# Optimization experiments

Measured on AMD Instinct MI355X. Metric: run time of the kernel, lower is better.

Reference implementation:

```python
import jax, jax.numpy as jnp
import numpy as np

N = 200000
D = 128
B = 8
VS = 0.4
XMIN, YMIN, ZMIN = -50.0, -50.0, -5.0
NX, NY, NZ = 250, 250, 20
VXYZ = NX * NY * NZ
FILL = np.int32(2_000_000_000)  # > any real voxel key, so padded uniques sort last
BN_EPS = 1e-5


def _bn(x, g, b, m, v):
    # BatchNorm1d in eval mode with given running stats
    return (x - m) * jax.lax.rsqrt(v + BN_EPS) * g + b


def _leaky(x):
    return jnp.where(x >= 0, x, 0.1 * x)


def setup_inputs() -> dict:
    key = jax.random.key(0)
    ks = jax.random.split(key, 12)
    points_feature = jax.random.normal(ks[0], (N, D), jnp.float32)
    u = jax.random.uniform(ks[1], (N, 3), jnp.float32)
    lo = jnp.array([XMIN, YMIN, ZMIN], jnp.float32)
    ext = jnp.array([100.0, 100.0, 8.0], jnp.float32)
    points_center = lo + 0.001 + u * (ext - 0.002)  # strictly inside pc_range
    batch_idx = jax.random.randint(ks[2], (N,), 0, B, jnp.int32)
    foreground_mask = jax.random.randint(ks[3], (N,), 0, 2, jnp.int32).astype(bool)
    timestamp = jax.random.normal(ks[4], (B,), jnp.float32) * 0.1
    w_pf = jax.random.normal(ks[5], (3 * D, D), jnp.float32) / np.sqrt(3 * D)
    b_pf = jax.random.normal(ks[6], (D,), jnp.float32) * 0.01
    g_pf = jax.random.uniform(ks[7], (D,), jnp.float32) + 0.5
    be_pf = jax.random.normal(ks[8], (D,), jnp.float32) * 0.1
    m_pf = jax.random.normal(ks[9], (D,), jnp.float32) * 0.1
    v_pf = jax.random.uniform(ks[10], (D,), jnp.float32) + 0.5
    ks2 = jax.random.split(ks[11], 6)
    w_cp = jax.random.normal(ks2[0], (D, D), jnp.float32) / np.sqrt(D)
    b_cp = jax.random.normal(ks2[1], (D,), jnp.float32) * 0.01
    g_cp = jax.random.uniform(ks2[2], (D,), jnp.float32) + 0.5
    be_cp = jax.random.normal(ks2[3], (D,), jnp.float32) * 0.1
    m_cp = jax.random.normal(ks2[4], (D,), jnp.float32) * 0.1
    v_cp = jax.random.uniform(ks2[5], (D,), jnp.float32) + 0.5
    return dict(points_feature=points_feature, points_center=points_center,
                batch_idx=batch_idx, foreground_mask=foreground_mask,
                timestamp=timestamp,
                w_pf=w_pf, b_pf=b_pf, g_pf=g_pf, be_pf=be_pf, m_pf=m_pf, v_pf=v_pf,
                w_cp=w_cp, b_cp=b_cp, g_cp=g_cp, be_cp=be_cp, m_cp=m_cp, v_cp=v_cp)


def reference(points_feature, points_center, batch_idx, foreground_mask, timestamp,
              w_pf, b_pf, g_pf, be_pf, m_pf, v_pf,
              w_cp, b_cp, g_cp, be_cp, m_cp, v_cp):
    # NOTE: the original forward computes a time position embedding and then
    # overwrites it with zeros_like, so its net contribution is exactly zero.
    n = points_feature.shape[0]
    # voxelize point centers -> (b, xi, yi, zi) encoded as a single int key
    xi = jnp.floor((points_center[:, 0] - XMIN) / VS).astype(jnp.int32)
    yi = jnp.floor((points_center[:, 1] - YMIN) / VS).astype(jnp.int32)
    zi = jnp.floor((points_center[:, 2] - ZMIN) / VS).astype(jnp.int32)
    vkey = ((batch_idx.astype(jnp.int32) * NX + xi) * NY + yi) * NZ + zi
    # torch.unique(dim=0) sorts lexicographically == sorted scalar keys
    uk, inv = jnp.unique(vkey, return_inverse=True, size=n, fill_value=FILL)
    fgf = foreground_mask.astype(points_feature.dtype)
    # K = points_cluster_idx_fore.max() + 1 (number of foreground clusters)
    K = jnp.max(jnp.where(foreground_mask, inv, -1)) + 1
    # scatter_mean of foreground point features per cluster (empty -> 0)
    cnt = jax.ops.segment_sum(fgf, inv, num_segments=n)
    csum = jax.ops.segment_sum(points_feature * fgf[:, None], inv, num_segments=n)
    cmean = csum / jnp.maximum(cnt, 1.0)[:, None]
    proj = _leaky(_bn(cmean @ w_cp + b_cp, g_cp, be_cp, m_cp, v_cp))
    valid = jnp.arange(n) < K
    # cluster_feature_all: rows < K hold projected cluster features, rest are 0
    cfa = jnp.where(valid[:, None], proj, 0.0)
    # associate voxels: halve the batch id (agent pairing), re-unique
    akey = (uk // VXYZ // 2) * VXYZ + uk % VXYZ
    _, ainv = jnp.unique(akey, return_inverse=True, size=n, fill_value=FILL)
    # scatter_mean of cluster features over associate voxels (only valid clusters)
    acnt = jax.ops.segment_sum(valid.astype(points_feature.dtype), ainv, num_segments=n)
    asum = jax.ops.segment_sum(cfa, ainv, num_segments=n)
    amean = asum / jnp.maximum(acnt, 1.0)[:, None]
    pf_assoc = amean[ainv[inv]]   # gather per point via voxel -> associate id
    pf_clu = cfa[inv]             # gather per point cluster feature
    amask = (pf_clu - pf_assoc).sum(axis=1) > 0
    cat = jnp.concatenate([points_feature, pf_clu, pf_assoc], axis=1)
    h = _leaky(_bn(cat @ w_pf + b_pf, g_pf, be_pf, m_pf, v_pf))
    newf = jnp.where(amask[:, None], h, points_feature)
    # original early-returns points_feature if associate_mask.sum() <= 1
    return jnp.where(amask.sum() > 1, newf, points_feature)
```

## Files before the change

kernel.cpp:

```cpp
#include <hip/hip_runtime.h>

#define SCAN_BS 256
#define SCAN_IT 16
#define SCAN_CHUNK (SCAN_BS * SCAN_IT)
#define NVOX 10000000
#define NAVOX 5000000
#define VXYZK 1250000

__device__ __forceinline__ float leakyf(float x) { return x >= 0.0f ? x : 0.1f * x; }

__global__ void k_init(int* c) {
  int t = threadIdx.x;
  if (t < 8) c[t] = (t == 2) ? -1 : 0;
}

__global__ void k_detect_fg(const unsigned* __restrict__ w, int nw, int* __restrict__ c) {
  int i = blockIdx.x * blockDim.x + threadIdx.x;
  if (i < nw && w[i] > 1u) atomicOr(&c[4], 1);
}

__device__ __forceinline__ int fg_get(const void* fgp, int i, int mode) {
  return mode ? (((const unsigned char*)fgp)[i] != 0) : (((const int*)fgp)[i] != 0);
}

__global__ void k_vkey(const float* __restrict__ pc, const int* __restrict__ bidx,
                       int* __restrict__ vkey, unsigned* __restrict__ dense, int N) {
  int i = blockIdx.x * blockDim.x + threadIdx.x;
  if (i >= N) return;
  float x = pc[3 * i], y = pc[3 * i + 1], z = pc[3 * i + 2];
  int xi = (int)floorf((x - (-50.0f)) / 0.4f);
  int yi = (int)floorf((y - (-50.0f)) / 0.4f);
  int zi = (int)floorf((z - (-5.0f)) / 0.4f);
  xi = min(max(xi, 0), 249); yi = min(max(yi, 0), 249); zi = min(max(zi, 0), 19);
  int b = min(max(bidx[i], 0), 7);
  int key = ((b * 250 + xi) * 250 + yi) * 20 + zi;
  vkey[i] = key;
  dense[key] = 1u;
}

__global__ void k_scan_block(unsigned* __restrict__ data, int n, unsigned* __restrict__ bsums) {
  __shared__ unsigned s[SCAN_BS];
  int tid = threadIdx.x;
  long base = (long)blockIdx.x * SCAN_CHUNK + (long)tid * SCAN_IT;
  unsigned v[SCAN_IT];
  unsigned tsum = 0;
#pragma unroll
  for (int j = 0; j < SCAN_IT; ++j) {
    long idx = base + j;
    v[j] = (idx < (long)n) ? data[idx] : 0u;
    tsum += v[j];
  }
  unsigned x = tsum;
  s[tid] = x;
  for (int off = 1; off < SCAN_BS; off <<= 1) {
    __syncthreads();
    unsigned y = (tid >= off) ? s[tid - off] : 0u;
    __syncthreads();
    x += y;
    s[tid] = x;
  }
  if (tid == SCAN_BS - 1) bsums[blockIdx.x] = x;
  unsigned run = x - tsum;
#pragma unroll
  for (int j = 0; j < SCAN_IT; ++j) {
    long idx = base + j;
    if (idx < (long)n) { data[idx] = run; run += v[j]; }
  }
}

__global__ void k_scan_sums(unsigned* __restrict__ data, int n, int* __restrict__ totalOut) {
  __shared__ unsigned s[SCAN_BS];
  int tid = threadIdx.x;
  int base = tid * SCAN_IT;
  unsigned v[SCAN_IT];
  unsigned tsum = 0;
#pragma unroll
  for (int j = 0; j < SCAN_IT; ++j) {
    int idx = base + j;
    v[j] = (idx < n) ? data[idx] : 0u;
    tsum += v[j];
  }
  unsigned x = tsum;
  s[tid] = x;
  for (int off = 1; off < SCAN_BS; off <<= 1) {
    __syncthreads();
    unsigned y = (tid >= off) ? s[tid - off] : 0u;
    __syncthreads();
    x += y;
    s[tid] = x;
  }
  if (tid == SCAN_BS - 1) *totalOut = (int)x;
  unsigned run = x - tsum;
#pragma unroll
  for (int j = 0; j < SCAN_IT; ++j) {
    int idx = base + j;
    if (idx < n) { data[idx] = run; run += v[j]; }
  }
}

__global__ void k_inv_ukey(const int* __restrict__ vkey, const unsigned* __restrict__ dense,
                           const unsigned* __restrict__ bsums, const void* __restrict__ fgp,
                           int* __restrict__ inv, int* __restrict__ ukey,
                           int* __restrict__ c, int N) {
  int i = blockIdx.x * blockDim.x + threadIdx.x;
  if (i >= N) return;
  int k = vkey[i];
  int r = (int)(dense[k] + bsums[k >> 12]);
  inv[i] = r;
  ukey[r] = k;
  if (fg_get(fgp, i, c[4])) atomicMax(&c[2], r);
}

__global__ void k_akey_mark(const int* __restrict__ ukey, int* __restrict__ akey,
                            unsigned* __restrict__ dense, const int* __restrict__ c, int N) {
  int r = blockIdx.x * blockDim.x + threadIdx.x;
  if (r >= N || r >= c[0]) return;
  int uk = ukey[r];
  int ak = (uk / VXYZK / 2) * VXYZK + uk % VXYZK;
  akey[r] = ak;
  dense[ak] = 1u;
}

__global__ void k_ainv(const int* __restrict__ akey, const unsigned* __restrict__ dense,
                       const unsigned* __restrict__ bsums, int* __restrict__ ainv,
                       const int* __restrict__ c, int N) {
  int r = blockIdx.x * blockDim.x + threadIdx.x;
  if (r >= N || r >= c[0]) return;
  int ak = akey[r];
  ainv[r] = (int)(dense[ak] + bsums[ak >> 12]);
}

__global__ void k_gcnt(const int* __restrict__ ainv_u, unsigned* __restrict__ gcnt,
                       const int* __restrict__ c, int N) {
  int r = blockIdx.x * blockDim.x + threadIdx.x;
  if (r >= N || r >= c[0]) return;
  atomicAdd(&gcnt[ainv_u[r]], 1u);
}

__global__ void k_build_lists(const int* __restrict__ ainv_u, const unsigned* __restrict__ gcnt,
                              int* __restrict__ mlist, int* __restrict__ nlist,
                              unsigned char* __restrict__ needp, int* __restrict__ c, int N) {
  int r = blockIdx.x * blockDim.x + threadIdx.x;
  if (r >= N || r >= c[0]) return;
  int g = ainv_u[r];
  if (gcnt[g] >= 2u) {
    int mp = atomicAdd(&c[5], 1);
    mlist[mp] = r;
    if (r <= c[2]) {
      needp[r] = 1;
      int np = atomicAdd(&c[6], 1);
      nlist[np] = r;
    }
  }
}

__global__ void k_zero_rows(const int* __restrict__ mlist, const int* __restrict__ ainv_u,
                            const int* __restrict__ c, float* __restrict__ csum,
                            float* __restrict__ asum) {
  int total = c[5] * 128;
  int stride = gridDim.x * blockDim.x;
  for (int idx = blockIdx.x * blockDim.x + threadIdx.x; idx < total; idx += stride) {
    int r = mlist[idx >> 7];
    int d = idx & 127;
    asum[(size_t)ainv_u[r] * 128 + d] = 0.0f;
    if (r <= c[2]) csum[(size_t)r * 128 + d] = 0.0f;
  }
}

__global__ void k_point_filter(const void* __restrict__ fgp, const int* __restrict__ inv,
                               const unsigned char* __restrict__ needp, float* __restrict__ cnt,
                               int* __restrict__ clist, int* __restrict__ c, int N) {
  int i = blockIdx.x * blockDim.x + threadIdx.x;
  if (i >= N) return;
  if (!fg_get(fgp, i, c[4])) return;
  int r = inv[i];
  if (!needp[r]) return;
  atomicAdd(&cnt[r], 1.0f);
  int p = atomicAdd(&c[7], 1);
  clist[p] = i;
}

__global__ void k_csum_accum(const float* __restrict__ pf, const int* __restrict__ clist,
                             const int* __restrict__ inv, float* __restrict__ csum,
                             const int* __restrict__ c) {
  int total = c[7] * 128;
  int stride = gridDim.x * blockDim.x;
  for (int idx = blockIdx.x * blockDim.x + threadIdx.x; idx < total; idx += stride) {
    int i = clist[idx >> 7];
    int d = idx & 127;
    int r = inv[i];
    atomicAdd(&csum[(size_t)r * 128 + d], pf[(size_t)i * 128 + d]);
  }
}

__global__ __launch_bounds__(128) void k_proj16(
    float* __restrict__ cs, const float* __restrict__ cnt, const int* __restrict__ nlist,
    const float* __restrict__ W, const float* __restrict__ bb,
    const float* __restrict__ gg, const float* __restrict__ be,
    const float* __restrict__ mm, const float* __restrict__ vv, const int* __restrict__ c) {
  int nc = c[6];
  int ntiles = (nc + 15) >> 4;
  __shared__ __align__(16) float tile[16][128];
  __shared__ int srow[16];
  int d = threadIdx.x;
  for (int tb = blockIdx.x; tb < ntiles; tb += gridDim.x) {
    int base = tb * 16;
    if (d < 16) srow[d] = (base + d < nc) ? nlist[base + d] : -1;
    __syncthreads();
    for (int p = 0; p < 16; ++p) {
      int r = srow[p];
      tile[p][d] = (r >= 0) ? cs[(size_t)r * 128 + d] / fmaxf(cnt[r], 1.0f) : 0.0f;
    }
    __syncthreads();
    float acc[16];
#pragma unroll
    for (int p = 0; p < 16; ++p) acc[p] = 0.0f;
    for (int k4 = 0; k4 < 32; ++k4) {
      float w0 = W[(4 * k4 + 0) * 128 + d];
      float w1 = W[(4 * k4 + 1) * 128 + d];
      float w2 = W[(4 * k4 + 2) * 128 + d];
      float w3 = W[(4 * k4 + 3) * 128 + d];
#pragma unroll
      for (int p = 0; p < 16; ++p) {
        float4 t4 = *(const float4*)&tile[p][4 * k4];
        acc[p] = fmaf(t4.x, w0, acc[p]);
        acc[p] = fmaf(t4.y, w1, acc[p]);
        acc[p] = fmaf(t4.z, w2, acc[p]);
        acc[p] = fmaf(t4.w, w3, acc[p]);
      }
    }
    float biasd = bb[d], scale = gg[d] / sqrtf(vv[d] + 1e-5f), md = mm[d], bed = be[d];
    for (int p = 0; p < 16; ++p) {
      int r = srow[p];
      if (r >= 0) {
        float pre = acc[p] + biasd;
        cs[(size_t)r * 128 + d] = leakyf((pre - md) * scale + bed);
      }
    }
    __syncthreads();
  }
}

__global__ void k_asum_accum(const float* __restrict__ cs, const int* __restrict__ nlist,
                             const int* __restrict__ ainv_u, float* __restrict__ asum,
                             float* __restrict__ acnt, const int* __restrict__ c) {
  int total = c[6] * 128;
  int stride = gridDim.x * blockDim.x;
  for (int idx = blockIdx.x * blockDim.x + threadIdx.x; idx < total; idx += stride) {
    int r = nlist[idx >> 7];
    int d = idx & 127;
    int g = ainv_u[r];
    atomicAdd(&asum[(size_t)g * 128 + d], cs[(size_t)r * 128 + d]);
    if (d == 0) atomicAdd(&acnt[g], 1.0f);
  }
}

__global__ void k_amask2(const float* __restrict__ cs, const float* __restrict__ asum,
                         const float* __restrict__ acnt, const int* __restrict__ ainv_u,
                         const int* __restrict__ mlist, const int* __restrict__ c,
                         unsigned* __restrict__ flag) {
  int mcount = c[5];
  int groups = gridDim.x * (blockDim.x >> 6);
  int j0 = blockIdx.x * (blockDim.x >> 6) + (threadIdx.x >> 6);
  int lane = threadIdx.x & 63;
  for (int j = j0; j < mcount; j += groups) {
    int r = mlist[j];
    int g = ainv_u[r];
    float mc = fmaxf(acnt[g], 1.0f);
    bool valid = r <= c[2];
    size_t rb = (size_t)r * 128, gb = (size_t)g * 128;
    float c0 = valid ? cs[rb + lane] : 0.0f;
    float c1 = valid ? cs[rb + 64 + lane] : 0.0f;
    float s = (c0 - asum[gb + lane] / mc) + (c1 - asum[gb + 64 + lane] / mc);
    for (int off = 32; off > 0; off >>= 1) s += __shfl_down(s, off);
    if (lane == 0) flag[r] = (s > 0.0f) ? 1u : 0u;
  }
}

__global__ void k_flagpts(const int* __restrict__ inv, const unsigned* __restrict__ flag,
                          int* __restrict__ plist, int* __restrict__ c, int N) {
  int i = blockIdx.x * blockDim.x + threadIdx.x;
  if (i >= N) return;
  if (flag[inv[i]]) {
    int p = atomicAdd(&c[3], 1);
    plist[p] = i;
  }
}

__global__ void k_copy(const float* __restrict__ pf, float* __restrict__ out, long n4) {
  long stride = (long)gridDim.x * blockDim.x;
  for (long idx = (long)blockIdx.x * blockDim.x + threadIdx.x; idx < n4; idx += stride) {
    ((float4*)out)[idx] = ((const float4*)pf)[idx];
  }
}

__global__ __launch_bounds__(128) void k_fgemm(
    const float* __restrict__ pf, const float* __restrict__ cs,
    const float* __restrict__ asum, const float* __restrict__ acnt,
    const int* __restrict__ inv, const int* __restrict__ ainv_u,
    const int* __restrict__ plist, const int* __restrict__ c,
    const float* __restrict__ W, const float* __restrict__ bb,
    const float* __restrict__ gg, const float* __restrict__ be,
    const float* __restrict__ mm, const float* __restrict__ vv,
    float* __restrict__ out) {
  int pcnt = c[3];
  if (pcnt <= 1) return;
  int ntiles = (pcnt + 15) >> 4;
  __shared__ __align__(16) float tile[16][384];
  __shared__ int si[16], sr[16], sg[16];
  __shared__ float smc[16];
  int t = threadIdx.x;
  int kmax = c[2];
  for (int tb = blockIdx.x; tb < ntiles; tb += gridDim.x) {
    int base = tb * 16;
    if (t < 16) {
      int i = (base + t < pcnt) ? plist[base + t] : -1;
      si[t] = i;
      int r = (i >= 0) ? inv[i] : 0;
      sr[t] = r;
      int g = ainv_u[r];
      sg[t] = g;
      smc[t] = fmaxf(acnt[g], 1.0f);
    }
    __syncthreads();
    for (int e = t; e < 16 * 96; e += 128) {
      int p = e / 96, f4 = e % 96;
      int i = si[p];
      float4 v = make_float4(0.f, 0.f, 0.f, 0.f);
      if (i >= 0) {
        if (f4 < 32) {
          v = ((const float4*)pf)[(size_t)i * 32 + f4];
        } else if (f4 < 64) {
          int r = sr[p];
          if (r <= kmax) v = ((const float4*)cs)[(size_t)r * 32 + (f4 - 32)];
        } else {
          float4 a = ((const float4*)asum)[(size_t)sg[p] * 32 + (f4 - 64)];
          float mc = smc[p];
          v = make_float4(a.x / mc, a.y / mc, a.z / mc, a.w / mc);
        }
      }
      *(float4*)&tile[p][f4 * 4] = v;
    }
    __syncthreads();
    float acc[16];
#pragma unroll
    for (int p = 0; p < 16; ++p) acc[p] = 0.0f;
    for (int k4 = 0; k4 < 96; ++k4) {
      float w0 = W[(4 * k4 + 0) * 128 + t];
      float w1 = W[(4 * k4 + 1) * 128 + t];
      float w2 = W[(4 * k4 + 2) * 128 + t];
      float w3 = W[(4 * k4 + 3) * 128 + t];
#pragma unroll
      for (int p = 0; p < 16; ++p) {
        float4 t4 = *(const float4*)&tile[p][4 * k4];
        acc[p] = fmaf(t4.x, w0, acc[p]);
        acc[p] = fmaf(t4.y, w1, acc[p]);
        acc[p] = fmaf(t4.z, w2, acc[p]);
        acc[p] = fmaf(t4.w, w3, acc[p]);
      }
    }
    float biasd = bb[t], scale = gg[t] / sqrtf(vv[t] + 1e-5f), md = mm[t], bed = be[t];
    for (int p = 0; p < 16; ++p) {
      int i = si[p];
      if (i >= 0) {
        float pre = acc[p] + biasd;
        out[(size_t)i * 128 + t] = leakyf((pre - md) * scale + bed);
      }
    }
    __syncthreads();
  }
}

extern "C" void kernel_launch(void* const* d_in, const int* in_sizes, int n_in,
                              void* d_out, int out_size, void* d_ws, size_t ws_size,
                              hipStream_t stream) {
  (void)n_in; (void)out_size; (void)ws_size;
  const float* pf   = (const float*)d_in[0];
  const float* pc   = (const float*)d_in[1];
  const int*   bidx = (const int*)d_in[2];
  const void*  fgp  = d_in[3];
  const float* Wpf  = (const float*)d_in[5];
  const float* bpf  = (const float*)d_in[6];
  const float* gpf  = (const float*)d_in[7];
  const float* bepf = (const float*)d_in[8];
  const float* mpf  = (const float*)d_in[9];
  const float* vpf  = (const float*)d_in[10];
  const float* Wcp  = (const float*)d_in[11];
  const float* bcp  = (const float*)d_in[12];
  const float* gcp  = (const float*)d_in[13];
  const float* becp = (const float*)d_in[14];
  const float* mcp  = (const float*)d_in[15];
  const float* vcp  = (const float*)d_in[16];
  float* out = (float*)d_out;
  int N = in_sizes[0] / 128;

  char* ws = (char*)d_ws;
  size_t o = 0;
  auto take = [&](size_t bytes) -> void* {
    void* p = ws + o;
    o += (bytes + 255) & ~(size_t)255;
    return p;
  };
  unsigned* dense  = (unsigned*)take((size_t)NVOX * 4);
  int* vkey        = (int*)take((size_t)N * 4);
  int* inv         = (int*)take((size_t)N * 4);
  int* ukey        = (int*)take((size_t)N * 4);
  int* akey        = (int*)take((size_t)N * 4);
  int* ainv_u      = (int*)take((size_t)N * 4);
  float* cnt       = (float*)take((size_t)N * 4);
  float* acnt      = (float*)take((size_t)N * 4);
  unsigned* flag   = (unsigned*)take((size_t)N * 4);
  unsigned* gcnt   = (unsigned*)take((size_t)N * 4);
  int* nlist       = (int*)take((size_t)N * 4);
  int* clist       = (int*)take((size_t)N * 4);
  unsigned char* needp = (unsigned char*)take((size_t)N);
  unsigned* bsums1 = (unsigned*)take((size_t)4096 * 4);
  unsigned* bsums2 = (unsigned*)take((size_t)4096 * 4);
  int* ctr         = (int*)take(256);
  float* csum      = (float*)take((size_t)N * 128 * 4);
  float* asum      = (float*)take((size_t)N * 128 * 4);
  int* mlist = vkey;
  int* plist = akey;

  hipMemsetAsync(dense, 0, (size_t)NVOX * 4, stream);
  hipMemsetAsync(cnt, 0, (size_t)N * 4, stream);
  hipMemsetAsync(acnt, 0, (size_t)N * 4, stream);
  hipMemsetAsync(flag, 0, (size_t)N * 4, stream);
  hipMemsetAsync(gcnt, 0, (size_t)N * 4, stream);
  hipMemsetAsync(needp, 0, (size_t)N, stream);
  k_init<<<1, 64, 0, stream>>>(ctr);

  int nb = (N + 255) / 256;
  int nw = N / 4;
  k_detect_fg<<<(nw + 255) / 256, 256, 0, stream>>>((const unsigned*)fgp, nw, ctr);
  k_vkey<<<nb, 256, 0, stream>>>(pc, bidx, vkey, dense, N);

  int blk1 = (NVOX + SCAN_CHUNK - 1) / SCAN_CHUNK;
  k_scan_block<<<blk1, SCAN_BS, 0, stream>>>(dense, NVOX, bsums1);
  k_scan_sums<<<1, SCAN_BS, 0, stream>>>(bsums1, blk1, &ctr[0]);
  k_inv_ukey<<<nb, 256, 0, stream>>>(vkey, dense, bsums1, fgp, inv, ukey, ctr, N);

  hipMemsetAsync(dense, 0, (size_t)NAVOX * 4, stream);
  k_akey_mark<<<nb, 256, 0, stream>>>(ukey, akey, dense, ctr, N);
  int blk2 = (NAVOX + SCAN_CHUNK - 1) / SCAN_CHUNK;
  k_scan_block<<<blk2, SCAN_BS, 0, stream>>>(dense, NAVOX, bsums2);
  k_scan_sums<<<1, SCAN_BS, 0, stream>>>(bsums2, blk2, &ctr[1]);
  k_ainv<<<nb, 256, 0, stream>>>(akey, dense, bsums2, ainv_u, ctr, N);

  k_gcnt<<<nb, 256, 0, stream>>>(ainv_u, gcnt, ctr, N);
  k_build_lists<<<nb, 256, 0, stream>>>(ainv_u, gcnt, mlist, nlist, needp, ctr, N);

  int gsw = 3125;
  k_zero_rows<<<gsw, 256, 0, stream>>>(mlist, ainv_u, ctr, csum, asum);
  k_point_filter<<<nb, 256, 0, stream>>>(fgp, inv, needp, cnt, clist, ctr, N);
  k_csum_accum<<<gsw, 256, 0, stream>>>(pf, clist, inv, csum, ctr);
  k_proj16<<<gsw, 128, 0, stream>>>(csum, cnt, nlist, Wcp, bcp, gcp, becp, mcp, vcp, ctr);
  k_asum_accum<<<gsw, 256, 0, stream>>>(csum, nlist, ainv_u, asum, acnt, ctr);
  k_amask2<<<1024, 256, 0, stream>>>(csum, asum, acnt, ainv_u, mlist, ctr, flag);
  k_flagpts<<<nb, 256, 0, stream>>>(inv, flag, plist, ctr, N);

  long n4 = (long)N * 32;
  k_copy<<<12800, 256, 0, stream>>>(pf, out, n4);
  k_fgemm<<<gsw, 128, 0, stream>>>(pf, csum, asum, acnt, inv, ainv_u, plist, ctr,
                                   Wpf, bpf, gpf, bepf, mpf, vpf, out);
}
```

Baseline: 582.2 us.

## Replace dense voxel occupancy arrays with bitsets and fuse small kernels

Voxel occupancy moves from 40MB/20MB dense uint arrays to bitsets with popcount-based word prefix scans and rank lookups. This shrinks the memset and scan traffic considerably. Several small kernels are fused: fg detection into vkey, gcnt into ainv, zero_rows with point_filter, and flagpts with copy. Memsets are collapsed into one contiguous region, the per-thread fg atomicMax becomes a wave reduction, and grid sizes are retuned.

After: 466.0 us. 20.0% less time.

```diff
diff --git a/kernel.cpp b/kernel.cpp
--- a/kernel.cpp
+++ b/kernel.cpp
@@ -5,27 +5,22 @@
 #define SCAN_CHUNK (SCAN_BS * SCAN_IT)
 #define NVOX 10000000
 #define NAVOX 5000000
+#define NWORDS1 312500
+#define NWORDS2 156250
 #define VXYZK 1250000
 
 __device__ __forceinline__ float leakyf(float x) { return x >= 0.0f ? x : 0.1f * x; }
-
-__global__ void k_init(int* c) {
-  int t = threadIdx.x;
-  if (t < 8) c[t] = (t == 2) ? -1 : 0;
-}
-
-__global__ void k_detect_fg(const unsigned* __restrict__ w, int nw, int* __restrict__ c) {
-  int i = blockIdx.x * blockDim.x + threadIdx.x;
-  if (i < nw && w[i] > 1u) atomicOr(&c[4], 1);
-}
 
 __device__ __forceinline__ int fg_get(const void* fgp, int i, int mode) {
   return mode ? (((const unsigned char*)fgp)[i] != 0) : (((const int*)fgp)[i] != 0);
 }
 
 __global__ void k_vkey(const float* __restrict__ pc, const int* __restrict__ bidx,
-                       int* __restrict__ vkey, unsigned* __restrict__ dense, int N) {
+                       const unsigned* __restrict__ fgw, int nw,
+                       int* __restrict__ vkey, unsigned* __restrict__ bits,
+                       int* __restrict__ c, int N) {
   int i = blockIdx.x * blockDim.x + threadIdx.x;
+  if (i < nw && fgw[i] > 1u) atomicOr(&c[4], 1);
   if (i >= N) return;
   float x = pc[3 * i], y = pc[3 * i + 1], z = pc[3 * i + 2];
   int xi = (int)floorf((x - (-50.0f)) / 0.4f);
@@ -35,10 +30,11 @@
   int b = min(max(bidx[i], 0), 7);
   int key = ((b * 250 + xi) * 250 + yi) * 20 + zi;
   vkey[i] = key;
-  dense[key] = 1u;
-}
-
-__global__ void k_scan_block(unsigned* __restrict__ data, int n, unsigned* __restrict__ bsums) {
+  atomicOr(&bits[key >> 5], 1u << (key & 31));
+}
+
+__global__ void k_scan_pop(const unsigned* __restrict__ bits, int nwords,
+                           unsigned* __restrict__ wordpfx, unsigned* __restrict__ bsums) {
   __shared__ unsigned s[SCAN_BS];
   int tid = threadIdx.x;
   long base = (long)blockIdx.x * SCAN_CHUNK + (long)tid * SCAN_IT;
@@ -47,7 +43,7 @@
 #pragma unroll
   for (int j = 0; j < SCAN_IT; ++j) {
     long idx = base + j;
-    v[j] = (idx < (long)n) ? data[idx] : 0u;
+    v[j] = (idx < (long)nwords) ? (unsigned)__popc(bits[idx]) : 0u;
     tsum += v[j];
   }
   unsigned x = tsum;
@@ -64,7 +60,7 @@
 #pragma unroll
   for (int j = 0; j < SCAN_IT; ++j) {
     long idx = base + j;
-    if (idx < (long)n) { data[idx] = run; run += v[j]; }
+    if (idx < (long)nwords) { wordpfx[idx] = run; run += v[j]; }
   }
 }
 
@@ -98,43 +94,50 @@
   }
 }
 
-__global__ void k_inv_ukey(const int* __restrict__ vkey, const unsigned* __restrict__ dense,
-                           const unsigned* __restrict__ bsums, const void* __restrict__ fgp,
-                           int* __restrict__ inv, int* __restrict__ ukey,
-                           int* __restrict__ c, int N) {
+__device__ __forceinline__ int rank_of(int key, const unsigned* bits,
+                                       const unsigned* wordpfx, const unsigned* bsums) {
+  int w = key >> 5, b = key & 31;
+  return (int)(wordpfx[w] + bsums[w >> 12] + (unsigned)__popc(bits[w] & ((1u << b) - 1u)));
+}
+
+__global__ void k_inv_ukey(const int* __restrict__ vkey, const unsigned* __restrict__ bits,
+                           const unsigned* __restrict__ wordpfx, const unsigned* __restrict__ bsums,
+                           const void* __restrict__ fgp, int* __restrict__ inv,
+                           int* __restrict__ ukey, int* __restrict__ c, int N) {
   int i = blockIdx.x * blockDim.x + threadIdx.x;
-  if (i >= N) return;
-  int k = vkey[i];
-  int r = (int)(dense[k] + bsums[k >> 12]);
-  inv[i] = r;
-  ukey[r] = k;
-  if (fg_get(fgp, i, c[4])) atomicMax(&c[2], r);
+  bool valid = i < N;
+  int mode = c[4];
+  int r = 0;
+  if (valid) {
+    int k = vkey[i];
+    r = rank_of(k, bits, wordpfx, bsums);
+    inv[i] = r;
+    ukey[r] = k;
+  }
+  int fgr = (valid && fg_get(fgp, i, mode)) ? r : -1;
+  for (int off = 32; off > 0; off >>= 1) fgr = max(fgr, __shfl_down(fgr, off));
+  if ((threadIdx.x & 63) == 0 && fgr >= 0) atomicMax(&c[2], fgr + 1);
 }
 
 __global__ void k_akey_mark(const int* __restrict__ ukey, int* __restrict__ akey,
-                            unsigned* __restrict__ dense, const int* __restrict__ c, int N) {
+                            unsigned* __restrict__ abits, const int* __restrict__ c, int N) {
   int r = blockIdx.x * blockDim.x + threadIdx.x;
   if (r >= N || r >= c[0]) return;
   int uk = ukey[r];
   int ak = (uk / VXYZK / 2) * VXYZK + uk % VXYZK;
   akey[r] = ak;
-  dense[ak] = 1u;
-}
-
-__global__ void k_ainv(const int* __restrict__ akey, const unsigned* __restrict__ dense,
-                       const unsigned* __restrict__ bsums, int* __restrict__ ainv,
+  atomicOr(&abits[ak >> 5], 1u << (ak & 31));
+}
+
+__global__ void k_ainv(const int* __restrict__ akey, const unsigned* __restrict__ abits,
+                       const unsigned* __restrict__ awordpfx, const unsigned* __restrict__ bsums,
+                       int* __restrict__ ainv, unsigned* __restrict__ gcnt,
                        const int* __restrict__ c, int N) {
   int r = blockIdx.x * blockDim.x + threadIdx.x;
   if (r >= N || r >= c[0]) return;
-  int ak = akey[r];
-  ainv[r] = (int)(dense[ak] + bsums[ak >> 12]);
-}
-
-__global__ void k_gcnt(const int* __restrict__ ainv_u, unsigned* __restrict__ gcnt,
-                       const int* __restrict__ c, int N) {
-  int r = blockIdx.x * blockDim.x + threadIdx.x;
-  if (r >= N || r >= c[0]) return;
-  atomicAdd(&gcnt[ainv_u[r]], 1u);
+  int g = rank_of(akey[r], abits, awordpfx, bsums);
+  ainv[r] = g;
+  atomicAdd(&gcnt[g], 1u);
 }
 
 __global__ void k_build_lists(const int* __restrict__ ainv_u, const unsigned* __restrict__ gcnt,
@@ -142,11 +145,10 @@
                               unsigned char* __restrict__ needp, int* __restrict__ c, int N) {
   int r = blockIdx.x * blockDim.x + threadIdx.x;
   if (r >= N || r >= c[0]) return;
-  int g = ainv_u[r];
-  if (gcnt[g] >= 2u) {
+  if (gcnt[ainv_u[r]] >= 2u) {
     int mp = atomicAdd(&c[5], 1);
     mlist[mp] = r;
-    if (r <= c[2]) {
+    if (r < c[2]) {
       needp[r] = 1;
       int np = atomicAdd(&c[6], 1);
       nlist[np] = r;
@@ -154,30 +156,31 @@
   }
 }
 
-__global__ void k_zero_rows(const int* __restrict__ mlist, const int* __restrict__ ainv_u,
-                            const int* __restrict__ c, float* __restrict__ csum,
-                            float* __restrict__ asum) {
-  int total = c[5] * 128;
+__global__ void k_zero_filter(const int* __restrict__ mlist, const int* __restrict__ ainv_u,
+                              const void* __restrict__ fgp, const int* __restrict__ inv,
+                              const unsigned char* __restrict__ needp,
+                              float* __restrict__ csum, float* __restrict__ asum,
+                              float* __restrict__ cnt, int* __restrict__ clist,
+                              int* __restrict__ c, int N) {
   int stride = gridDim.x * blockDim.x;
-  for (int idx = blockIdx.x * blockDim.x + threadIdx.x; idx < total; idx += stride) {
+  int tid0 = blockIdx.x * blockDim.x + threadIdx.x;
+  int K = c[2];
+  int totalA = c[5] * 128;
+  for (int idx = tid0; idx < totalA; idx += stride) {
     int r = mlist[idx >> 7];
     int d = idx & 127;
     asum[(size_t)ainv_u[r] * 128 + d] = 0.0f;
-    if (r <= c[2]) csum[(size_t)r * 128 + d] = 0.0f;
-  }
-}
-
-__global__ void k_point_filter(const void* __restrict__ fgp, const int* __restrict__ inv,
-                               const unsigned char* __restrict__ needp, float* __restrict__ cnt,
-                               int* __restrict__ clist, int* __restrict__ c, int N) {
-  int i = blockIdx.x * blockDim.x + threadIdx.x;
-  if (i >= N) return;
-  if (!fg_get(fgp, i, c[4])) return;
-  int r = inv[i];
-  if (!needp[r]) return;
-  atomicAdd(&cnt[r], 1.0f);
-  int p = atomicAdd(&c[7], 1);
-  clist[p] = i;
+    if (r < K) csum[(size_t)r * 128 + d] = 0.0f;
+  }
+  int mode = c[4];
+  for (int i = tid0; i < N; i += stride) {
+    if (!fg_get(fgp, i, mode)) continue;
+    int r = inv[i];
+    if (!needp[r]) continue;
+    atomicAdd(&cnt[r], 1.0f);
+    int p = atomicAdd(&c[7], 1);
+    clist[p] = i;
+  }
 }
 
 __global__ void k_csum_accum(const float* __restrict__ pf, const int* __restrict__ clist,
@@ -188,8 +191,7 @@
   for (int idx = blockIdx.x * blockDim.x + threadIdx.x; idx < total; idx += stride) {
     int i = clist[idx >> 7];
     int d = idx & 127;
-    int r = inv[i];
-    atomicAdd(&csum[(size_t)r * 128 + d], pf[(size_t)i * 128 + d]);
+    atomicAdd(&csum[(size_t)inv[i] * 128 + d], pf[(size_t)i * 128 + d]);
   }
 }
 
@@ -263,11 +265,12 @@
   int groups = gridDim.x * (blockDim.x >> 6);
   int j0 = blockIdx.x * (blockDim.x >> 6) + (threadIdx.x >> 6);
   int lane = threadIdx.x & 63;
+  int K = c[2];
   for (int j = j0; j < mcount; j += groups) {
     int r = mlist[j];
     int g = ainv_u[r];
     float mc = fmaxf(acnt[g], 1.0f);
-    bool valid = r <= c[2];
+    bool valid = r < K;
     size_t rb = (size_t)r * 128, gb = (size_t)g * 128;
     float c0 = valid ? cs[rb + lane] : 0.0f;
     float c1 = valid ? cs[rb + 64 + lane] : 0.0f;
@@ -277,19 +280,19 @@
   }
 }
 
-__global__ void k_flagpts(const int* __restrict__ inv, const unsigned* __restrict__ flag,
-                          int* __restrict__ plist, int* __restrict__ c, int N) {
-  int i = blockIdx.x * blockDim.x + threadIdx.x;
-  if (i >= N) return;
-  if (flag[inv[i]]) {
-    int p = atomicAdd(&c[3], 1);
-    plist[p] = i;
-  }
-}
-
-__global__ void k_copy(const float* __restrict__ pf, float* __restrict__ out, long n4) {
+__global__ void k_copy_flag(const float* __restrict__ pf, const int* __restrict__ inv,
+                            const unsigned* __restrict__ flag, float* __restrict__ out,
+                            int* __restrict__ plist, int* __restrict__ c, int N) {
   long stride = (long)gridDim.x * blockDim.x;
-  for (long idx = (long)blockIdx.x * blockDim.x + threadIdx.x; idx < n4; idx += stride) {
+  long tid0 = (long)blockIdx.x * blockDim.x + threadIdx.x;
+  for (long i = tid0; i < (long)N; i += stride) {
+    if (flag[inv[i]]) {
+      int p = atomicAdd(&c[3], 1);
+      plist[p] = (int)i;
+    }
+  }
+  long n4 = (long)N * 32;
+  for (long idx = tid0; idx < n4; idx += stride) {
     ((float4*)out)[idx] = ((const float4*)pf)[idx];
   }
 }
@@ -305,12 +308,12 @@
     float* __restrict__ out) {
   int pcnt = c[3];
   if (pcnt <= 1) return;
+  int K = c[2];
   int ntiles = (pcnt + 15) >> 4;
   __shared__ __align__(16) float tile[16][384];
   __shared__ int si[16], sr[16], sg[16];
   __shared__ float smc[16];
   int t = threadIdx.x;
-  int kmax = c[2];
   for (int tb = blockIdx.x; tb < ntiles; tb += gridDim.x) {
     int base = tb * 16;
     if (t < 16) {
@@ -332,7 +335,7 @@
           v = ((const float4*)pf)[(size_t)i * 32 + f4];
         } else if (f4 < 64) {
           int r = sr[p];
-          if (r <= kmax) v = ((const float4*)cs)[(size_t)r * 32 + (f4 - 32)];
+          if (r < K) v = ((const float4*)cs)[(size_t)r * 32 + (f4 - 32)];
         } else {
           float4 a = ((const float4*)asum)[(size_t)sg[p] * 32 + (f4 - 64)];
           float mc = smc[p];
@@ -401,66 +404,57 @@
     o += (bytes + 255) & ~(size_t)255;
     return p;
   };
-  unsigned* dense  = (unsigned*)take((size_t)NVOX * 4);
+  unsigned* bits   = (unsigned*)take((size_t)NWORDS1 * 4);
+  unsigned* abits  = (unsigned*)take((size_t)NWORDS2 * 4);
+  float* cnt       = (float*)take((size_t)N * 4);
+  float* acnt      = (float*)take((size_t)N * 4);
+  unsigned* flag   = (unsigned*)take((size_t)N * 4);
+  unsigned* gcnt   = (unsigned*)take((size_t)N * 4);
+  unsigned char* needp = (unsigned char*)take((size_t)N);
+  int* ctr         = (int*)take(256);
+  size_t zeroBytes = o;
+  unsigned* wordpfx  = (unsigned*)take((size_t)NWORDS1 * 4);
+  unsigned* awordpfx = (unsigned*)take((size_t)NWORDS2 * 4);
+  unsigned* bsums1 = (unsigned*)take((size_t)4096 * 4);
+  unsigned* bsums2 = (unsigned*)take((size_t)4096 * 4);
   int* vkey        = (int*)take((size_t)N * 4);
   int* inv         = (int*)take((size_t)N * 4);
   int* ukey        = (int*)take((size_t)N * 4);
   int* akey        = (int*)take((size_t)N * 4);
   int* ainv_u      = (int*)take((size_t)N * 4);
-  float* cnt       = (float*)take((size_t)N * 4);
-  float* acnt      = (float*)take((size_t)N * 4);
-  unsigned* flag   = (unsigned*)take((size_t)N * 4);
-  unsigned* gcnt   = (unsigned*)take((size_t)N * 4);
   int* nlist       = (int*)take((size_t)N * 4);
   int* clist       = (int*)take((size_t)N * 4);
-  unsigned char* needp = (unsigned char*)take((size_t)N);
-  unsigned* bsums1 = (unsigned*)take((size_t)4096 * 4);
-  unsigned* bsums2 = (unsigned*)take((size_t)4096 * 4);
-  int* ctr         = (int*)take(256);
   float* csum      = (float*)take((size_t)N * 128 * 4);
   float* asum      = (float*)take((size_t)N * 128 * 4);
   int* mlist = vkey;
   int* plist = akey;
 
-  hipMemsetAsync(dense, 0, (size_t)NVOX * 4, stream);
-  hipMemsetAsync(cnt, 0, (size_t)N * 4, stream);
-  hipMemsetAsync(acnt, 0, (size_t)N * 4, stream);
-  hipMemsetAsync(flag, 0, (size_t)N * 4, stream);
-  hipMemsetAsync(gcnt, 0, (size_t)N * 4, stream);
-  hipMemsetAsync(needp, 0, (size_t)N, stream);
-  k_init<<<1, 64, 0, stream>>>(ctr);
+  hipMemsetAsync(ws, 0, zeroBytes, stream);
 
   int nb = (N + 255) / 256;
   int nw = N / 4;
-  k_detect_fg<<<(nw + 255) / 256, 256, 0, stream>>>((const unsigned*)fgp, nw, ctr);
-  k_vkey<<<nb, 256, 0, stream>>>(pc, bidx, vkey, dense, N);
-
-  int blk1 = (NVOX + SCAN_CHUNK - 1) / SCAN_CHUNK;
-  k_scan_block<<<blk1, SCAN_BS, 0, stream>>>(dense, NVOX, bsums1);
+  k_vkey<<<nb, 256, 0, stream>>>(pc, bidx, (const unsigned*)fgp, nw, vkey, bits, ctr, N);
+
+  int blk1 = (NWORDS1 + SCAN_CHUNK - 1) / SCAN_CHUNK;
+  k_scan_pop<<<blk1, SCAN_BS, 0, stream>>>(bits, NWORDS1, wordpfx, bsums1);
   k_scan_sums<<<1, SCAN_BS, 0, stream>>>(bsums1, blk1, &ctr[0]);
-  k_inv_ukey<<<nb, 256, 0, stream>>>(vkey, dense, bsums1, fgp, inv, ukey, ctr, N);
-
-  hipMemsetAsync(dense, 0, (size_t)NAVOX * 4, stream);
-  k_akey_mark<<<nb, 256, 0, stream>>>(ukey, akey, dense, ctr, N);
-  int blk2 = (NAVOX + SCAN_CHUNK - 1) / SCAN_CHUNK;
-  k_scan_block<<<blk2, SCAN_BS, 0, stream>>>(dense, NAVOX, bsums2);
+  k_inv_ukey<<<nb, 256, 0, stream>>>(vkey, bits, wordpfx, bsums1, fgp, inv, ukey, ctr, N);
+
+  k_akey_mark<<<nb, 256, 0, stream>>>(ukey, akey, abits, ctr, N);
+  int blk2 = (NWORDS2 + SCAN_CHUNK - 1) / SCAN_CHUNK;
+  k_scan_pop<<<blk2, SCAN_BS, 0, stream>>>(abits, NWORDS2, awordpfx, bsums2);
   k_scan_sums<<<1, SCAN_BS, 0, stream>>>(bsums2, blk2, &ctr[1]);
-  k_ainv<<<nb, 256, 0, stream>>>(akey, dense, bsums2, ainv_u, ctr, N);
-
-  k_gcnt<<<nb, 256, 0, stream>>>(ainv_u, gcnt, ctr, N);
+  k_ainv<<<nb, 256, 0, stream>>>(akey, abits, awordpfx, bsums2, ainv_u, gcnt, ctr, N);
+
   k_build_lists<<<nb, 256, 0, stream>>>(ainv_u, gcnt, mlist, nlist, needp, ctr, N);
-
-  int gsw = 3125;
-  k_zero_rows<<<gsw, 256, 0, stream>>>(mlist, ainv_u, ctr, csum, asum);
-  k_point_filter<<<nb, 256, 0, stream>>>(fgp, inv, needp, cnt, clist, ctr, N);
-  k_csum_accum<<<gsw, 256, 0, stream>>>(pf, clist, inv, csum, ctr);
-  k_proj16<<<gsw, 128, 0, stream>>>(csum, cnt, nlist, Wcp, bcp, gcp, becp, mcp, vcp, ctr);
-  k_asum_accum<<<gsw, 256, 0, stream>>>(csum, nlist, ainv_u, asum, acnt, ctr);
-  k_amask2<<<1024, 256, 0, stream>>>(csum, asum, acnt, ainv_u, mlist, ctr, flag);
-  k_flagpts<<<nb, 256, 0, stream>>>(inv, flag, plist, ctr, N);
-
-  long n4 = (long)N * 32;
-  k_copy<<<12800, 256, 0, stream>>>(pf, out, n4);
-  k_fgemm<<<gsw, 128, 0, stream>>>(pf, csum, asum, acnt, inv, ainv_u, plist, ctr,
-                                   Wpf, bpf, gpf, bepf, mpf, vpf, out);
-}
+  k_zero_filter<<<1024, 256, 0, stream>>>(mlist, ainv_u, fgp, inv, needp,
+                                          csum, asum, cnt, clist, ctr, N);
+  k_csum_accum<<<1024, 256, 0, stream>>>(pf, clist, inv, csum, ctr);
+  k_proj16<<<512, 128, 0, stream>>>(csum, cnt, nlist, Wcp, bcp, gcp, becp, mcp, vcp, ctr);
+  k_asum_accum<<<512, 256, 0, stream>>>(csum, nlist, ainv_u, asum, acnt, ctr);
+  k_amask2<<<512, 256, 0, stream>>>(csum, asum, acnt, ainv_u, mlist, ctr, flag);
+
+  k_copy_flag<<<4096, 256, 0, stream>>>(pf, inv, flag, out, plist, ctr, N);
+  k_fgemm<<<1024, 128, 0, stream>>>(pf, csum, asum, acnt, inv, ainv_u, plist, ctr,
+                                    Wpf, bpf, gpf, bepf, mpf, vpf, out);
+}
```
